# Kernel optimization log

Measured on AMD Instinct MI355X. Metric: run time of the kernel, lower is better.

## Reference

```python
import jax, jax.numpy as jnp
import numpy as np

# TokenLearner 1.1 (RT-1 variant): grouped 1x1-conv MLP attention + weighted spatial mean pool.
# Grouped 1x1 convs == per-group matmuls, so we avoid materializing the g-times repeated input.

def setup_inputs() -> dict:
    key = jax.random.key(0)
    k1, k2, k3, k4, k5 = jax.random.split(key, 5)
    B, C, H, W = 32, 768, 16, 16
    G, FF = 8, 2
    D = C * FF  # inner channels per group = 1536
    x = jax.random.normal(k1, (B, C, H, W), dtype=jnp.float32)
    # conv1: groups=G, in per group = C, out per group = D
    W1 = jax.random.normal(k2, (G, D, C), dtype=jnp.float32) * (1.0 / np.sqrt(C))
    b1 = jax.random.normal(k3, (G, D), dtype=jnp.float32) * 0.02
    # conv2: groups=G, in per group = D, out per group = 1
    W2 = jax.random.normal(k4, (G, D), dtype=jnp.float32) * (1.0 / np.sqrt(D))
    b2 = jax.random.normal(k5, (G,), dtype=jnp.float32) * 0.02
    return {"x": x, "W1": W1, "b1": b1, "W2": W2, "b2": b2}


def reference(x, W1, b1, W2, b2):
    # x: [B,C,H,W]. Per-group first projection (grouped 1x1 conv on repeated x):
    # h1[b,g,d,h,w] = sum_c W1[g,d,c] * x[b,c,h,w] + b1[g,d]
    h1 = jnp.einsum('gdc,bchw->bgdhw', W1, x) + b1[None, :, :, None, None]
    h1 = jax.nn.gelu(h1, approximate=False)  # nn.GELU default is exact erf
    # second grouped 1x1 conv -> one attention logit per group
    attn = jnp.einsum('gd,bgdhw->bghw', W2, h1) + b2[None, :, None, None]
    # weighted mean pool: out[b,c,g] = mean_{h,w} x[b,c,h,w] * attn[b,g,h,w]
    Hs, Ws = x.shape[2], x.shape[3]
    out = jnp.einsum('bchw,bghw->bcg', x, attn) / (Hs * Ws)
    return out
```

## Files before the change

### kernel.cpp

```cpp
#include <hip/hip_runtime.h>
#include <hip/hip_bf16.h>
#include <cstdint>
#include <cstddef>

typedef __bf16 bf16_t;
typedef __bf16 bf16x8 __attribute__((ext_vector_type(8)));
typedef __bf16 bf16x4 __attribute__((ext_vector_type(4)));
typedef float  f32x4  __attribute__((ext_vector_type(4)));
typedef float  f32x16 __attribute__((ext_vector_type(16)));

#define AS1(p) ((const __attribute__((address_space(1))) unsigned int*)(p))
#define AS3(p) ((__attribute__((address_space(3))) unsigned int*)(p))

#if __has_builtin(__builtin_amdgcn_rcpf)
  #define FAST_RCP(x) __builtin_amdgcn_rcpf(x)
#else
  #define FAST_RCP(x) (1.0f / (x))
#endif

__device__ __forceinline__ float gelu_fast(float v) {
    float z = fabsf(v) * 0.70710678118654752440f;
    float t = FAST_RCP(fmaf(0.3275911f, z, 1.0f));
    float p = fmaf(t, 1.061405429f, -1.453152027f);
    p = fmaf(t, p, 1.421413741f);
    p = fmaf(t, p, -0.284496736f);
    p = fmaf(t, p, 0.254829592f);
    p *= t;
    float e = p * exp2f(-z * z * 1.4426950408889634f);
    float phi = (v >= 0.0f) ? fmaf(-0.5f, e, 1.0f) : (0.5f * e);
    return v * phi;
}

__global__ void k_prep(const float* __restrict__ W1, bf16_t* __restrict__ W1bf,
                       const float* __restrict__ x, bf16_t* __restrict__ xT,
                       float* __restrict__ attn) {
    __shared__ bf16_t t[64][66];
    int bx = blockIdx.x;
    int tid = threadIdx.x;
    if (bx < 9216) {
        int i = bx * 256 + tid;
        f32x4 v = ((const f32x4*)W1)[i];
        bf16x4 o;
        o[0] = (bf16_t)v[0]; o[1] = (bf16_t)v[1];
        o[2] = (bf16_t)v[2]; o[3] = (bf16_t)v[3];
        ((bf16x4*)W1bf)[i] = o;
        return;
    }
    if (bx >= 10752) {
        int i = (bx - 10752) * 256 + tid;
        ((f32x4*)attn)[i] = f32x4{0.f, 0.f, 0.f, 0.f};
        return;
    }
    int bx2 = bx - 9216;
    int ct = bx2 % 12, ht = (bx2 / 12) % 4, b = bx2 / 48;
    int col = tid & 63, rr = tid >> 6;
    const float* xb = x + ((size_t)b * 768 + (size_t)ct * 64) * 256 + ht * 64;
    #pragma unroll
    for (int r = 0; r < 16; ++r) {
        int c = r * 4 + rr;
        t[c][col] = (bf16_t)xb[(size_t)c * 256 + col];
    }
    __syncthreads();
    bf16_t* xTb = xT + ((size_t)b * 256 + (size_t)ht * 64) * 768 + ct * 64;
    #pragma unroll
    for (int r = 0; r < 16; ++r) {
        int hw = r * 4 + rr;
        xTb[(size_t)hw * 768 + col] = t[col][hw];
    }
}

__global__ __launch_bounds__(512) void k_attn_gemm(
    const bf16_t* __restrict__ W1bf, const bf16_t* __restrict__ xTbf,
    const float* __restrict__ b1, const float* __restrict__ W2,
    float* __restrict__ attn)
{
    extern __shared__ char smem[];
    float* attn_s = (float*)(smem + 98304);

    const int tid = threadIdx.x;
    const int l = tid & 63, w = tid >> 6;
    const int wm = w >> 2, wn = w & 3;
    const int bid = blockIdx.x;
    const int g     = bid & 7;
    const int local = bid >> 3;
    const int chunk = local / 24;
    const int sub   = local % 24;
    const int mt    = sub >> 1;
    const int b     = chunk * 2 + (sub & 1);

    const bf16_t* gAk = W1bf + ((size_t)g * 1536 + (size_t)mt * 128) * 768;
    const bf16_t* gBk = xTbf + (size_t)b * 256 * 768;

    if (tid < 256) attn_s[tid] = 0.0f;

    int voffA[2], ldsA[2], voffB[4], ldsB[4];
    #pragma unroll
    for (int i = 0; i < 2; ++i) {
        int q = i * 512 + tid, row = q >> 3, sc = (q & 7) ^ (row & 7);
        voffA[i] = row * 768 + sc * 8;
        ldsA[i] = q * 16;
    }
    #pragma unroll
    for (int i = 0; i < 4; ++i) {
        int q = i * 512 + tid, row = q >> 3, sc = (q & 7) ^ (row & 7);
        voffB[i] = row * 768 + sc * 8;
        ldsB[i] = q * 16;
    }

    const int hi = l >> 5;
    uint32_t aoff[4][2], boff[4][2];
    #pragma unroll
    for (int ks = 0; ks < 4; ++ks) {
        const int c = ks * 2 + hi;
        #pragma unroll
        for (int mi = 0; mi < 2; ++mi) {
            int r = wm * 64 + mi * 32 + (l & 31);
            aoff[ks][mi] = (uint32_t)((r * 8 + (c ^ (r & 7))) * 16);
        }
        #pragma unroll
        for (int ni = 0; ni < 2; ++ni) {
            int r = wn * 64 + ni * 32 + (l & 31);
            boff[ks][ni] = (uint32_t)((r * 8 + (c ^ (r & 7))) * 16);
        }
    }

    f32x16 acc[2][2];
    #pragma unroll
    for (int mi = 0; mi < 2; ++mi)
        #pragma unroll
        for (int ni = 0; ni < 2; ++ni)
            acc[mi][ni] = (f32x16)(0.0f);

    auto STAGE = [&](int abase, int bbase) {
        #pragma unroll
        for (int i = 0; i < 2; ++i)
            __builtin_amdgcn_global_load_lds(AS1(gAk + voffA[i]),
                AS3(smem + abase + ldsA[i]), 16, 0, 0);
        #pragma unroll
        for (int i = 0; i < 4; ++i)
            __builtin_amdgcn_global_load_lds(AS1(gBk + voffB[i]),
                AS3(smem + bbase + ldsB[i]), 16, 0, 0);
        gAk += 64; gBk += 64;
    };

    auto COMPUTE = [&](int abase, int bbase) {
        #pragma unroll
        for (int ks = 0; ks < 4; ++ks) {
            bf16x8 af[2], bfr[2];
            #pragma unroll
            for (int mi = 0; mi < 2; ++mi)
                af[mi] = *(const bf16x8*)(smem + abase + aoff[ks][mi]);
            #pragma unroll
            for (int ni = 0; ni < 2; ++ni)
                bfr[ni] = *(const bf16x8*)(smem + bbase + boff[ks][ni]);
            #pragma unroll
            for (int mi = 0; mi < 2; ++mi)
                #pragma unroll
                for (int ni = 0; ni < 2; ++ni)
                    acc[mi][ni] = __builtin_amdgcn_mfma_f32_32x32x16_bf16(
                        af[mi], bfr[ni], acc[mi][ni], 0, 0, 0);
        }
    };

    STAGE(0, 32768);
    #pragma unroll 1
    for (int kt2 = 0; kt2 < 5; ++kt2) {
        STAGE(16384, 65536);
        asm volatile("s_waitcnt vmcnt(6)" ::: "memory");
        __builtin_amdgcn_s_barrier();
        COMPUTE(0, 32768);
        __builtin_amdgcn_s_barrier();
        STAGE(0, 32768);
        asm volatile("s_waitcnt vmcnt(6)" ::: "memory");
        __builtin_amdgcn_s_barrier();
        COMPUTE(16384, 65536);
        __builtin_amdgcn_s_barrier();
    }
    STAGE(16384, 65536);
    asm volatile("s_waitcnt vmcnt(6)" ::: "memory");
    __builtin_amdgcn_s_barrier();
    COMPUTE(0, 32768);
    asm volatile("s_waitcnt vmcnt(0)" ::: "memory");
    __builtin_amdgcn_s_barrier();
    COMPUTE(16384, 65536);

    float partial[2] = {0.f, 0.f};
    #pragma unroll
    for (int mi = 0; mi < 2; ++mi) {
        const int dbase = g * 1536 + mt * 128 + wm * 64 + mi * 32 + hi * 4;
        #pragma unroll
        for (int rq = 0; rq < 4; ++rq) {
            f32x4 b1v = *(const f32x4*)&b1[dbase + rq * 8];
            f32x4 w2v = *(const f32x4*)&W2[dbase + rq * 8];
            #pragma unroll
            for (int j = 0; j < 4; ++j) {
                const int rg = rq * 4 + j;
                #pragma unroll
                for (int ni = 0; ni < 2; ++ni) {
                    float h = acc[mi][ni][rg] + b1v[j];
                    partial[ni] += gelu_fast(h) * w2v[j];
                }
            }
        }
    }
    #pragma unroll
    for (int ni = 0; ni < 2; ++ni)
        partial[ni] += __shfl_xor(partial[ni], 32, 64);
    if (l < 32) {
        #pragma unroll
        for (int ni = 0; ni < 2; ++ni)
            atomicAdd(&attn_s[wn * 64 + ni * 32 + l], partial[ni]);
    }
    __syncthreads();
    if (tid < 256)
        atomicAdd(&attn[((size_t)b * 8 + g) * 256 + tid], attn_s[tid]);
}

__global__ void k_pool(const float* __restrict__ x, const float* __restrict__ attn,
                       const float* __restrict__ b2, float* __restrict__ out)
{
    int tid = threadIdx.x;
    int l = tid & 63, w = tid >> 6;
    int gidx = blockIdx.x * 4 + w;
    int b = gidx / 768;
    f32x4 xv = ((const f32x4*)(x + (size_t)gidx * 256))[l];
    float accg[8];
    #pragma unroll
    for (int g = 0; g < 8; ++g) {
        f32x4 av = ((const f32x4*)(attn + ((size_t)b * 8 + g) * 256))[l];
        float bb = b2[g];
        accg[g] = xv[0] * (av[0] + bb) + xv[1] * (av[1] + bb)
                + xv[2] * (av[2] + bb) + xv[3] * (av[3] + bb);
    }
    #pragma unroll
    for (int g = 0; g < 8; ++g) {
        accg[g] += __shfl_xor(accg[g], 32, 64);
        accg[g] += __shfl_xor(accg[g], 16, 64);
        accg[g] += __shfl_xor(accg[g], 8, 64);
        accg[g] += __shfl_xor(accg[g], 4, 64);
        accg[g] += __shfl_xor(accg[g], 2, 64);
        accg[g] += __shfl_xor(accg[g], 1, 64);
    }
    if (l == 0) {
        #pragma unroll
        for (int g = 0; g < 8; ++g)
            out[(size_t)gidx * 8 + g] = accg[g] * (1.0f / 256.0f);
    }
}

extern "C" void kernel_launch(void* const* d_in, const int* in_sizes, int n_in,
                              void* d_out, int out_size, void* d_ws, size_t ws_size,
                              hipStream_t stream) {
    const float* x  = (const float*)d_in[0];
    const float* W1 = (const float*)d_in[1];
    const float* b1 = (const float*)d_in[2];
    const float* W2 = (const float*)d_in[3];
    const float* b2 = (const float*)d_in[4];
    float* out = (float*)d_out;

    char* ws = (char*)d_ws;
    bf16_t* W1bf = (bf16_t*)ws;
    bf16_t* xTbf = (bf16_t*)(ws + 18874368);
    float*  attn = (float*)(ws + 18874368 + 12582912);

    hipFuncSetAttribute((const void*)k_attn_gemm,
                        hipFuncAttributeMaxDynamicSharedMemorySize, 99328);

    k_prep<<<dim3(10816), dim3(256), 0, stream>>>(W1, W1bf, x, xTbf, attn);
    k_attn_gemm<<<dim3(3072), dim3(512), 99328, stream>>>(W1bf, xTbf, b1, W2, attn);
    k_pool<<<dim3(6144), dim3(256), 0, stream>>>(x, attn, b2, out);
}
```

Before: 317.0 us.

## Triple-buffer GEMM K-loop with split staging and prioritized MFMA phases

Replaces the double-buffered LDS pipeline in the attention GEMM with a three-stage ring buffer. Each stage's global-to-LDS loads are split across two half-phases and interleaved with fragment reads and MFMA bursts, which are raised with s_setprio. The aim is to hide load latency better and keep the matrix units busy. LDS use grows from about 97KB to 145KB per block, which may cut occupancy, and the hand-tuned vmcnt and barrier scheme is fragile.

```diff
diff --git a/kernel.cpp b/kernel.cpp
--- a/kernel.cpp
+++ b/kernel.cpp
@@ -75,7 +75,7 @@
     float* __restrict__ attn)
 {
     extern __shared__ char smem[];
-    float* attn_s = (float*)(smem + 98304);
+    float* attn_s = (float*)(smem + 147456);
 
     const int tid = threadIdx.x;
     const int l = tid & 63, w = tid >> 6;
@@ -88,8 +88,8 @@
     const int mt    = sub >> 1;
     const int b     = chunk * 2 + (sub & 1);
 
-    const bf16_t* gAk = W1bf + ((size_t)g * 1536 + (size_t)mt * 128) * 768;
-    const bf16_t* gBk = xTbf + (size_t)b * 256 * 768;
+    const bf16_t* gAs = W1bf + ((size_t)g * 1536 + (size_t)mt * 128) * 768;
+    const bf16_t* gBs = xTbf + (size_t)b * 256 * 768;
 
     if (tid < 256) attn_s[tid] = 0.0f;
 
@@ -131,58 +131,72 @@
         for (int ni = 0; ni < 2; ++ni)
             acc[mi][ni] = (f32x16)(0.0f);
 
-    auto STAGE = [&](int abase, int bbase) {
-        #pragma unroll
-        for (int i = 0; i < 2; ++i)
-            __builtin_amdgcn_global_load_lds(AS1(gAk + voffA[i]),
-                AS3(smem + abase + ldsA[i]), 16, 0, 0);
-        #pragma unroll
-        for (int i = 0; i < 4; ++i)
-            __builtin_amdgcn_global_load_lds(AS1(gBk + voffB[i]),
-                AS3(smem + bbase + ldsB[i]), 16, 0, 0);
-        gAk += 64; gBk += 64;
+    auto STAGE_H1 = [&](int sb) {
+        __builtin_amdgcn_global_load_lds(AS1(gAs + voffA[0]),
+            AS3(smem + sb + ldsA[0]), 16, 0, 0);
+        __builtin_amdgcn_global_load_lds(AS1(gAs + voffA[1]),
+            AS3(smem + sb + ldsA[1]), 16, 0, 0);
+        __builtin_amdgcn_global_load_lds(AS1(gBs + voffB[0]),
+            AS3(smem + sb + 16384 + ldsB[0]), 16, 0, 0);
     };
-
-    auto COMPUTE = [&](int abase, int bbase) {
-        #pragma unroll
-        for (int ks = 0; ks < 4; ++ks) {
-            bf16x8 af[2], bfr[2];
-            #pragma unroll
-            for (int mi = 0; mi < 2; ++mi)
-                af[mi] = *(const bf16x8*)(smem + abase + aoff[ks][mi]);
+    auto STAGE_H2 = [&](int sb) {
+        #pragma unroll
+        for (int i = 1; i < 4; ++i)
+            __builtin_amdgcn_global_load_lds(AS1(gBs + voffB[i]),
+                AS3(smem + sb + 16384 + ldsB[i]), 16, 0, 0);
+        gAs += 64; gBs += 64;
+    };
+
+    auto PHASE = [&](int cb, int k2, bool do_stage, int sb, int half) {
+        bf16x8 fa0[2], fb0[2], fa1[2], fb1[2];
+        #pragma unroll
+        for (int mi = 0; mi < 2; ++mi)
+            fa0[mi] = *(const bf16x8*)(smem + cb + aoff[k2 * 2][mi]);
+        #pragma unroll
+        for (int ni = 0; ni < 2; ++ni)
+            fb0[ni] = *(const bf16x8*)(smem + cb + 16384 + boff[k2 * 2][ni]);
+        #pragma unroll
+        for (int mi = 0; mi < 2; ++mi)
+            fa1[mi] = *(const bf16x8*)(smem + cb + aoff[k2 * 2 + 1][mi]);
+        #pragma unroll
+        for (int ni = 0; ni < 2; ++ni)
+            fb1[ni] = *(const bf16x8*)(smem + cb + 16384 + boff[k2 * 2 + 1][ni]);
+        if (do_stage) { if (half == 0) STAGE_H1(sb); else STAGE_H2(sb); }
+        __builtin_amdgcn_s_barrier();
+        __builtin_amdgcn_s_setprio(1);
+        #pragma unroll
+        for (int mi = 0; mi < 2; ++mi)
             #pragma unroll
             for (int ni = 0; ni < 2; ++ni)
-                bfr[ni] = *(const bf16x8*)(smem + bbase + boff[ks][ni]);
+                acc[mi][ni] = __builtin_amdgcn_mfma_f32_32x32x16_bf16(
+                    fa0[mi], fb0[ni], acc[mi][ni], 0, 0, 0);
+        #pragma unroll
+        for (int mi = 0; mi < 2; ++mi)
             #pragma unroll
-            for (int mi = 0; mi < 2; ++mi)
-                #pragma unroll
-                for (int ni = 0; ni < 2; ++ni)
-                    acc[mi][ni] = __builtin_amdgcn_mfma_f32_32x32x16_bf16(
-                        af[mi], bfr[ni], acc[mi][ni], 0, 0, 0);
-        }
+            for (int ni = 0; ni < 2; ++ni)
+                acc[mi][ni] = __builtin_amdgcn_mfma_f32_32x32x16_bf16(
+                    fa1[mi], fb1[ni], acc[mi][ni], 0, 0, 0);
+        __builtin_amdgcn_s_setprio(0);
     };
 
-    STAGE(0, 32768);
-    #pragma unroll 1
-    for (int kt2 = 0; kt2 < 5; ++kt2) {
-        STAGE(16384, 65536);
-        asm volatile("s_waitcnt vmcnt(6)" ::: "memory");
-        __builtin_amdgcn_s_barrier();
-        COMPUTE(0, 32768);
-        __builtin_amdgcn_s_barrier();
-        STAGE(0, 32768);
-        asm volatile("s_waitcnt vmcnt(6)" ::: "memory");
-        __builtin_amdgcn_s_barrier();
-        COMPUTE(16384, 65536);
-        __builtin_amdgcn_s_barrier();
-    }
-    STAGE(16384, 65536);
+    STAGE_H1(0);      STAGE_H2(0);
+    STAGE_H1(49152);  STAGE_H2(49152);
     asm volatile("s_waitcnt vmcnt(6)" ::: "memory");
     __builtin_amdgcn_s_barrier();
-    COMPUTE(0, 32768);
-    asm volatile("s_waitcnt vmcnt(0)" ::: "memory");
-    __builtin_amdgcn_s_barrier();
-    COMPUTE(16384, 65536);
+
+    #pragma unroll
+    for (int t = 0; t < 12; ++t) {
+        const int cb = (t % 3) * 49152;
+        const int sb = ((t + 2) % 3) * 49152;
+        const bool st = (t < 10);
+
+        PHASE(cb, 0, st, sb, 0);
+        __builtin_amdgcn_s_barrier();
+        PHASE(cb, 1, st, sb, 1);
+        if (t < 10)       asm volatile("s_waitcnt vmcnt(6)" ::: "memory");
+        else if (t == 10) asm volatile("s_waitcnt vmcnt(0)" ::: "memory");
+        __builtin_amdgcn_s_barrier();
+    }
 
     float partial[2] = {0.f, 0.f};
     #pragma unroll
@@ -264,9 +278,9 @@
     float*  attn = (float*)(ws + 18874368 + 12582912);
 
     hipFuncSetAttribute((const void*)k_attn_gemm,
-                        hipFuncAttributeMaxDynamicSharedMemorySize, 99328);
+                        hipFuncAttributeMaxDynamicSharedMemorySize, 148480);
 
     k_prep<<<dim3(10816), dim3(256), 0, stream>>>(W1, W1bf, x, xTbf, attn);
-    k_attn_gemm<<<dim3(3072), dim3(512), 99328, stream>>>(W1bf, xTbf, b1, W2, attn);
+    k_attn_gemm<<<dim3(3072), dim3(512), 148480, stream>>>(W1bf, xTbf, b1, W2, attn);
     k_pool<<<dim3(6144), dim3(256), 0, stream>>>(x, attn, b2, out);
 }
```

Result: slower. 354.5 us (+11.8%).

## Pre-pack W1 into MFMA fragment layout and load A directly to registers

Applied to the files above, without the earlier changes.

The prep kernel now writes W1 in bf16 in a layout pre-tiled to match the 32x32x16 MFMA A-fragment, so each lane fetches its A operand with one 16-byte global load and A no longer passes through LDS. Only the activation B tile is staged in LDS with double buffering. The block tile grows to 256x256 (each wave handles 64x128), the grid is halved, and launch bounds ask for two blocks per CU. The aim is less LDS traffic and more reuse per block, at the cost of exposed global-load latency on A fetches and higher register pressure from eight accumulators.

```diff
diff --git a/kernel.cpp b/kernel.cpp
--- a/kernel.cpp
+++ b/kernel.cpp
@@ -31,27 +31,36 @@
     return v * phi;
 }
 
-__global__ void k_prep(const float* __restrict__ W1, bf16_t* __restrict__ W1bf,
+__global__ void k_prep(const float* __restrict__ W1, bf16_t* __restrict__ Apack,
                        const float* __restrict__ x, bf16_t* __restrict__ xT,
                        float* __restrict__ attn) {
     __shared__ bf16_t t[64][66];
     int bx = blockIdx.x;
     int tid = threadIdx.x;
-    if (bx < 9216) {
+    if (bx < 4608) {
         int i = bx * 256 + tid;
-        f32x4 v = ((const f32x4*)W1)[i];
-        bf16x4 o;
-        o[0] = (bf16_t)v[0]; o[1] = (bf16_t)v[1];
-        o[2] = (bf16_t)v[2]; o[3] = (bf16_t)v[3];
-        ((bf16x4*)W1bf)[i] = o;
+        int kc = i % 96;
+        int dg = i / 96;
+        int d = dg % 1536, g = dg / 1536;
+        const float* src = W1 + (size_t)dg * 768 + kc * 8;
+        f32x4 v0 = *(const f32x4*)src;
+        f32x4 v1 = *(const f32x4*)(src + 4);
+        bf16x8 o;
+        o[0] = (bf16_t)v0[0]; o[1] = (bf16_t)v0[1];
+        o[2] = (bf16_t)v0[2]; o[3] = (bf16_t)v0[3];
+        o[4] = (bf16_t)v1[0]; o[5] = (bf16_t)v1[1];
+        o[6] = (bf16_t)v1[2]; o[7] = (bf16_t)v1[3];
+        size_t dst = ((size_t)(g * 48 + (d >> 5)) * 48 + (kc >> 1)) * 512
+                   + ((d & 31) + 32 * (kc & 1)) * 8;
+        *(bf16x8*)(Apack + dst) = o;
         return;
     }
-    if (bx >= 10752) {
-        int i = (bx - 10752) * 256 + tid;
+    if (bx >= 6144) {
+        int i = (bx - 6144) * 256 + tid;
         ((f32x4*)attn)[i] = f32x4{0.f, 0.f, 0.f, 0.f};
         return;
     }
-    int bx2 = bx - 9216;
+    int bx2 = bx - 4608;
     int ct = bx2 % 12, ht = (bx2 / 12) % 4, b = bx2 / 48;
     int col = tid & 63, rr = tid >> 6;
     const float* xb = x + ((size_t)b * 768 + (size_t)ct * 64) * 256 + ht * 64;
@@ -69,37 +78,31 @@
     }
 }
 
-__global__ __launch_bounds__(512) void k_attn_gemm(
-    const bf16_t* __restrict__ W1bf, const bf16_t* __restrict__ xTbf,
+__global__ __launch_bounds__(512, 2) void k_attn_gemm(
+    const bf16_t* __restrict__ Apack, const bf16_t* __restrict__ xTbf,
     const float* __restrict__ b1, const float* __restrict__ W2,
     float* __restrict__ attn)
 {
     extern __shared__ char smem[];
-    float* attn_s = (float*)(smem + 98304);
+    float* attn_s = (float*)(smem + 65536);
 
     const int tid = threadIdx.x;
     const int l = tid & 63, w = tid >> 6;
-    const int wm = w >> 2, wn = w & 3;
+    const int wm = w >> 1, wn = w & 1;
     const int bid = blockIdx.x;
     const int g     = bid & 7;
     const int local = bid >> 3;
-    const int chunk = local / 24;
-    const int sub   = local % 24;
+    const int chunk = local / 12;
+    const int sub   = local % 12;
     const int mt    = sub >> 1;
     const int b     = chunk * 2 + (sub & 1);
 
-    const bf16_t* gAk = W1bf + ((size_t)g * 1536 + (size_t)mt * 128) * 768;
-    const bf16_t* gBk = xTbf + (size_t)b * 256 * 768;
+    const bf16_t* gB = xTbf + (size_t)b * 256 * 768;
+    const bf16_t* pA = Apack + ((size_t)(g * 48 + mt * 8 + wm * 2) * 48) * 512 + l * 8;
 
     if (tid < 256) attn_s[tid] = 0.0f;
 
-    int voffA[2], ldsA[2], voffB[4], ldsB[4];
-    #pragma unroll
-    for (int i = 0; i < 2; ++i) {
-        int q = i * 512 + tid, row = q >> 3, sc = (q & 7) ^ (row & 7);
-        voffA[i] = row * 768 + sc * 8;
-        ldsA[i] = q * 16;
-    }
+    int voffB[4]; int ldsB[4];
     #pragma unroll
     for (int i = 0; i < 4; ++i) {
         int q = i * 512 + tid, row = q >> 3, sc = (q & 7) ^ (row & 7);
@@ -108,86 +111,60 @@
     }
 
     const int hi = l >> 5;
-    uint32_t aoff[4][2], boff[4][2];
-    #pragma unroll
-    for (int ks = 0; ks < 4; ++ks) {
-        const int c = ks * 2 + hi;
-        #pragma unroll
-        for (int mi = 0; mi < 2; ++mi) {
-            int r = wm * 64 + mi * 32 + (l & 31);
-            aoff[ks][mi] = (uint32_t)((r * 8 + (c ^ (r & 7))) * 16);
+    uint32_t boff[4][4];
+    #pragma unroll
+    for (int s = 0; s < 4; ++s) {
+        const int c = s * 2 + hi;
+        #pragma unroll
+        for (int ni = 0; ni < 4; ++ni) {
+            int r = wn * 128 + ni * 32 + (l & 31);
+            boff[s][ni] = (uint32_t)((r * 8 + (c ^ (r & 7))) * 16);
         }
-        #pragma unroll
-        for (int ni = 0; ni < 2; ++ni) {
-            int r = wn * 64 + ni * 32 + (l & 31);
-            boff[ks][ni] = (uint32_t)((r * 8 + (c ^ (r & 7))) * 16);
+    }
+
+    f32x16 acc[2][4];
+    #pragma unroll
+    for (int mi = 0; mi < 2; ++mi)
+        #pragma unroll
+        for (int ni = 0; ni < 4; ++ni)
+            acc[mi][ni] = (f32x16)(0.0f);
+
+    auto STAGE = [&](int bufbase, int t) {
+        #pragma unroll
+        for (int i = 0; i < 4; ++i)
+            __builtin_amdgcn_global_load_lds(AS1(gB + voffB[i] + t * 64),
+                AS3(smem + bufbase + ldsB[i]), 16, 0, 0);
+    };
+
+    STAGE(0, 0);
+    #pragma unroll
+    for (int t = 0; t < 12; ++t) {
+        __syncthreads();
+        if (t < 11) STAGE(((t + 1) & 1) * 32768, t + 1);
+        const int bufb = (t & 1) * 32768;
+        #pragma unroll
+        for (int s = 0; s < 4; ++s) {
+            bf16x8 a0 = *(const bf16x8*)(pA + (t * 4 + s) * 512);
+            bf16x8 a1 = *(const bf16x8*)(pA + 48 * 512 + (t * 4 + s) * 512);
+            bf16x8 bb[4];
+            #pragma unroll
+            for (int ni = 0; ni < 4; ++ni)
+                bb[ni] = *(const bf16x8*)(smem + bufb + boff[s][ni]);
+            #pragma unroll
+            for (int ni = 0; ni < 4; ++ni)
+                acc[0][ni] = __builtin_amdgcn_mfma_f32_32x32x16_bf16(
+                    a0, bb[ni], acc[0][ni], 0, 0, 0);
+            #pragma unroll
+            for (int ni = 0; ni < 4; ++ni)
+                acc[1][ni] = __builtin_amdgcn_mfma_f32_32x32x16_bf16(
+                    a1, bb[ni], acc[1][ni], 0, 0, 0);
         }
     }
 
-    f32x16 acc[2][2];
-    #pragma unroll
-    for (int mi = 0; mi < 2; ++mi)
-        #pragma unroll
-        for (int ni = 0; ni < 2; ++ni)
-            acc[mi][ni] = (f32x16)(0.0f);
-
-    auto STAGE = [&](int abase, int bbase) {
-        #pragma unroll
-        for (int i = 0; i < 2; ++i)
-            __builtin_amdgcn_global_load_lds(AS1(gAk + voffA[i]),
-                AS3(smem + abase + ldsA[i]), 16, 0, 0);
-        #pragma unroll
-        for (int i = 0; i < 4; ++i)
-            __builtin_amdgcn_global_load_lds(AS1(gBk + voffB[i]),
-                AS3(smem + bbase + ldsB[i]), 16, 0, 0);
-        gAk += 64; gBk += 64;
-    };
-
-    auto COMPUTE = [&](int abase, int bbase) {
-        #pragma unroll
-        for (int ks = 0; ks < 4; ++ks) {
-            bf16x8 af[2], bfr[2];
-            #pragma unroll
-            for (int mi = 0; mi < 2; ++mi)
-                af[mi] = *(const bf16x8*)(smem + abase + aoff[ks][mi]);
-            #pragma unroll
-            for (int ni = 0; ni < 2; ++ni)
-                bfr[ni] = *(const bf16x8*)(smem + bbase + boff[ks][ni]);
-            #pragma unroll
-            for (int mi = 0; mi < 2; ++mi)
-                #pragma unroll
-                for (int ni = 0; ni < 2; ++ni)
-                    acc[mi][ni] = __builtin_amdgcn_mfma_f32_32x32x16_bf16(
-                        af[mi], bfr[ni], acc[mi][ni], 0, 0, 0);
-        }
-    };
-
-    STAGE(0, 32768);
-    #pragma unroll 1
-    for (int kt2 = 0; kt2 < 5; ++kt2) {
-        STAGE(16384, 65536);
-        asm volatile("s_waitcnt vmcnt(6)" ::: "memory");
-        __builtin_amdgcn_s_barrier();
-        COMPUTE(0, 32768);
-        __builtin_amdgcn_s_barrier();
-        STAGE(0, 32768);
-        asm volatile("s_waitcnt vmcnt(6)" ::: "memory");
-        __builtin_amdgcn_s_barrier();
-        COMPUTE(16384, 65536);
-        __builtin_amdgcn_s_barrier();
-    }
-    STAGE(16384, 65536);
-    asm volatile("s_waitcnt vmcnt(6)" ::: "memory");
-    __builtin_amdgcn_s_barrier();
-    COMPUTE(0, 32768);
-    asm volatile("s_waitcnt vmcnt(0)" ::: "memory");
-    __builtin_amdgcn_s_barrier();
-    COMPUTE(16384, 65536);
-
-    float partial[2] = {0.f, 0.f};
+    float partial[4] = {0.f, 0.f, 0.f, 0.f};
     #pragma unroll
     for (int mi = 0; mi < 2; ++mi) {
-        const int dbase = g * 1536 + mt * 128 + wm * 64 + mi * 32 + hi * 4;
+        const int dbase = g * 1536 + mt * 256 + wm * 64 + mi * 32 + hi * 4;
         #pragma unroll
         for (int rq = 0; rq < 4; ++rq) {
             f32x4 b1v = *(const f32x4*)&b1[dbase + rq * 8];
@@ -196,7 +173,7 @@
             for (int j = 0; j < 4; ++j) {
                 const int rg = rq * 4 + j;
                 #pragma unroll
-                for (int ni = 0; ni < 2; ++ni) {
+                for (int ni = 0; ni < 4; ++ni) {
                     float h = acc[mi][ni][rg] + b1v[j];
                     partial[ni] += gelu_fast(h) * w2v[j];
                 }
@@ -204,12 +181,12 @@
         }
     }
     #pragma unroll
-    for (int ni = 0; ni < 2; ++ni)
+    for (int ni = 0; ni < 4; ++ni)
         partial[ni] += __shfl_xor(partial[ni], 32, 64);
     if (l < 32) {
         #pragma unroll
-        for (int ni = 0; ni < 2; ++ni)
-            atomicAdd(&attn_s[wn * 64 + ni * 32 + l], partial[ni]);
+        for (int ni = 0; ni < 4; ++ni)
+            atomicAdd(&attn_s[wn * 128 + ni * 32 + l], partial[ni]);
     }
     __syncthreads();
     if (tid < 256)
@@ -259,14 +236,14 @@
     float* out = (float*)d_out;
 
     char* ws = (char*)d_ws;
-    bf16_t* W1bf = (bf16_t*)ws;
-    bf16_t* xTbf = (bf16_t*)(ws + 18874368);
-    float*  attn = (float*)(ws + 18874368 + 12582912);
+    bf16_t* Apack = (bf16_t*)ws;
+    bf16_t* xTbf  = (bf16_t*)(ws + 18874368);
+    float*  attn  = (float*)(ws + 18874368 + 12582912);
 
     hipFuncSetAttribute((const void*)k_attn_gemm,
-                        hipFuncAttributeMaxDynamicSharedMemorySize, 99328);
-
-    k_prep<<<dim3(10816), dim3(256), 0, stream>>>(W1, W1bf, x, xTbf, attn);
-    k_attn_gemm<<<dim3(3072), dim3(512), 99328, stream>>>(W1bf, xTbf, b1, W2, attn);
+                        hipFuncAttributeMaxDynamicSharedMemorySize, 66560);
+
+    k_prep<<<dim3(6208), dim3(256), 0, stream>>>(W1, Apack, x, xTbf, attn);
+    k_attn_gemm<<<dim3(1536), dim3(512), 66560, stream>>>(Apack, xTbf, b1, W2, attn);
     k_pool<<<dim3(6144), dim3(256), 0, stream>>>(x, attn, b2, out);
 }
```

New measurement: 333.9 us. 1.05x slower.
